# Kernel tuning notes

Hardware: AMD Instinct MI355X
Metric: run time of the kernel (lower is better)

Reference implementation:

```python
import jax, jax.numpy as jnp
import numpy as np

ALPHA = 1.702
LIMIT = 7.0
EPS = 1e-5

E, K, H, I = 8, 2, 2048, 2048
B, S = 1, 1024


def setup_inputs() -> dict:
    key = jax.random.key(0)
    k1, k2, k3, k4, k5 = jax.random.split(key, 5)
    x = jax.random.normal(k1, (B, S, H), dtype=jnp.float32)
    norm_w = jax.random.normal(k2, (H,), dtype=jnp.float32) * 0.02 + 1.0
    router_w = jax.random.normal(k3, (E, H), dtype=jnp.float32) * (1.0 / np.sqrt(H))
    w_gu = jax.random.normal(k4, (E, H, 2 * I), dtype=jnp.float32) * (1.0 / np.sqrt(H))
    w_down = jax.random.normal(k5, (E, I, H), dtype=jnp.float32) * (1.0 / np.sqrt(I))
    return {"x": x, "norm_w": norm_w, "router_w": router_w,
            "w_gu": w_gu, "w_down": w_down, "top_k": K}


def _rmsnorm(x, w):
    var = jnp.mean(x * x, axis=-1, keepdims=True)
    return x * jax.lax.rsqrt(var + EPS) * w


def _swiglu(h):
    # interleaved gate/linear halves, clamped (GPT-OSS style)
    glu = jnp.minimum(h[..., ::2], LIMIT)
    lin = jnp.clip(h[..., 1::2], -LIMIT, LIMIT)
    return glu * jax.nn.sigmoid(ALPHA * glu) * (lin + 1.0)


def reference(x, norm_w, router_w, w_gu, w_down, top_k):
    b, s, h = x.shape
    t = _rmsnorm(x, norm_w).reshape(b * s, h)          # [T, H]
    T = t.shape[0]

    # Router: linear -> softmax -> top-k -> normalize selected affinities
    logits = jnp.einsum('th,eh->te', t, router_w)      # [T, E]
    probs = jax.nn.softmax(logits, axis=-1)
    vals, idx = jax.lax.top_k(probs, top_k)            # [T, K]
    vals = vals / jnp.sum(vals, axis=-1, keepdims=True)
    cw = jnp.zeros_like(probs).at[jnp.arange(T)[:, None], idx].add(vals)  # [T, E]

    # Expert MLPs (dense per-expert reference of the blockwise grouped GEMM)
    hgu = jnp.einsum('th,ehf->etf', t, w_gu)           # [E, T, 2I]
    act = _swiglu(hgu)                                 # [E, T, I]
    oe = jnp.einsum('eti,eio->eto', act, w_down)       # [E, T, H]
    out = jnp.einsum('eto,te->to', oe, cw)             # [T, H]
    return out.reshape(b, s, h)
```

## Files before the change

kernel.cpp:

```cpp
#include <hip/hip_runtime.h>
#include <hip/hip_bf16.h>

#define H_   2048
#define E_   8
#define T_   1024
#define TWOI 4096
#define I_   2048
#define ALPHA 1.702f
#define LIMIT 7.0f

#define BM 128
#define BN 128
#define BKK 32
#define BTW 40

typedef __attribute__((ext_vector_type(8))) short short8;
typedef __attribute__((ext_vector_type(4))) float f32x4;

#define AS3U(p) ((__attribute__((address_space(3))) unsigned int*)(p))
#define AS1U(p) ((const __attribute__((address_space(1))) unsigned int*)(p))

__device__ __forceinline__ unsigned short f2bf(float f) {
    unsigned int u = __float_as_uint(f);
    u += 0x7fff + ((u >> 16) & 1);
    return (unsigned short)(u >> 16);
}

__device__ __forceinline__ unsigned int cvtpk_bf16(float lo, float hi) {
    unsigned int r;
    asm("v_cvt_pk_bf16_f32 %0, %1, %2" : "=v"(r) : "v"(lo), "v"(hi));
    return r;
}

__global__ void zero_counts(int* __restrict__ counts) {
    int i = threadIdx.x;
    if (i < E_) counts[i] = 0;
}

__global__ __launch_bounds__(256) void rms_router(
    const float* __restrict__ x, const float* __restrict__ nw,
    const float* __restrict__ rw,
    unsigned short* __restrict__ tbf, int* __restrict__ counts,
    int* __restrict__ tlist, int* __restrict__ tslot, float* __restrict__ tw)
{
    int t = blockIdx.x;
    int tid = threadIdx.x;
    int wave = tid >> 6, lane = tid & 63;
    const float* xr = x + (size_t)t * H_;

    float4 v0 = *(const float4*)(xr + tid * 4);
    float4 v1 = *(const float4*)(xr + 1024 + tid * 4);
    float ss = v0.x*v0.x + v0.y*v0.y + v0.z*v0.z + v0.w*v0.w
             + v1.x*v1.x + v1.y*v1.y + v1.z*v1.z + v1.w*v1.w;
    #pragma unroll
    for (int s = 32; s; s >>= 1) ss += __shfl_xor(ss, s);

    __shared__ float red[4];
    __shared__ float wlog[4][8];
    if (lane == 0) red[wave] = ss;
    __syncthreads();
    float total = red[0] + red[1] + red[2] + red[3];
    float scale = rsqrtf(total * (1.0f / H_) + 1e-5f);

    float4 n0 = *(const float4*)(nw + tid * 4);
    float4 n1 = *(const float4*)(nw + 1024 + tid * 4);
    float tv[8];
    tv[0] = v0.x * scale * n0.x; tv[1] = v0.y * scale * n0.y;
    tv[2] = v0.z * scale * n0.z; tv[3] = v0.w * scale * n0.w;
    tv[4] = v1.x * scale * n1.x; tv[5] = v1.y * scale * n1.y;
    tv[6] = v1.z * scale * n1.z; tv[7] = v1.w * scale * n1.w;

    ushort4 o0 = make_ushort4(f2bf(tv[0]), f2bf(tv[1]), f2bf(tv[2]), f2bf(tv[3]));
    ushort4 o1 = make_ushort4(f2bf(tv[4]), f2bf(tv[5]), f2bf(tv[6]), f2bf(tv[7]));
    *(ushort4*)(tbf + (size_t)t * H_ + tid * 4) = o0;
    *(ushort4*)(tbf + (size_t)t * H_ + 1024 + tid * 4) = o1;

    float acc[E_];
    #pragma unroll
    for (int e = 0; e < E_; e++) {
        const float* r0 = rw + (size_t)e * H_ + tid * 4;
        float4 a = *(const float4*)r0;
        float4 b = *(const float4*)(r0 + 1024);
        acc[e] = tv[0]*a.x + tv[1]*a.y + tv[2]*a.z + tv[3]*a.w
               + tv[4]*b.x + tv[5]*b.y + tv[6]*b.z + tv[7]*b.w;
    }
    #pragma unroll
    for (int s = 32; s; s >>= 1)
        #pragma unroll
        for (int e = 0; e < E_; e++) acc[e] += __shfl_xor(acc[e], s);
    if (lane == 0)
        #pragma unroll
        for (int e = 0; e < E_; e++) wlog[wave][e] = acc[e];
    __syncthreads();

    if (tid == 0) {
        float lg[E_];
        #pragma unroll
        for (int e = 0; e < E_; e++)
            lg[e] = wlog[0][e] + wlog[1][e] + wlog[2][e] + wlog[3][e];
        int i0 = 0;
        #pragma unroll
        for (int e = 1; e < E_; e++) if (lg[e] > lg[i0]) i0 = e;
        int i1 = -1;
        #pragma unroll
        for (int e = 0; e < E_; e++) {
            if (e == i0) continue;
            if (i1 < 0 || lg[e] > lg[i1]) i1 = e;
        }
        float e1 = expf(lg[i1] - lg[i0]);
        float s = 1.0f + e1;
        float w0 = 1.0f / s, w1 = e1 / s;
        int p0 = atomicAdd(&counts[i0], 1);
        tlist[i0 * T_ + p0] = t; tslot[i0 * T_ + p0] = 0; tw[i0 * T_ + p0] = w0;
        int p1 = atomicAdd(&counts[i1], 1);
        tlist[i1 * T_ + p1] = t; tslot[i1 * T_ + p1] = 1; tw[i1 * T_ + p1] = w1;
    }
}

__device__ __forceinline__ void compute_step(
    const unsigned short (*Asb)[BKK], const unsigned short (*Btb)[BTW],
    int wm, int wn, int lane, f32x4 acc[4][4])
{
    short8 a[4], b[4];
    int arow = wm * 64 + (lane & 15);
    int brow = wn * 64 + (lane & 15);
    int koff = (lane >> 4) * 8;
    #pragma unroll
    for (int mi = 0; mi < 4; mi++)
        a[mi] = *(const short8*)(&Asb[arow + mi * 16][koff]);
    #pragma unroll
    for (int ni = 0; ni < 4; ni++)
        b[ni] = *(const short8*)(&Btb[brow + ni * 16][koff]);
    __builtin_amdgcn_s_setprio(1);
    #pragma unroll
    for (int mi = 0; mi < 4; mi++)
        #pragma unroll
        for (int ni = 0; ni < 4; ni++)
            acc[mi][ni] = __builtin_amdgcn_mfma_f32_16x16x32_bf16(a[mi], b[ni], acc[mi][ni], 0, 0, 0);
    __builtin_amdgcn_s_setprio(0);
}

#define STEP(TT, RCUR, RNEXT, PRE) {                                               \
    if (PRE) {                                                                     \
        int kk2_ = ((TT) + 2) * BKK;                                               \
        __builtin_amdgcn_global_load_lds(AS1U(asrc0 + kk2_), AS3U(&As[c2][wave * 32][0]), 16, 0, 0);      \
        __builtin_amdgcn_global_load_lds(AS1U(asrc1 + kk2_), AS3U(&As[c2][wave * 32 + 16][0]), 16, 0, 0); \
        _Pragma("unroll")                                                          \
        for (int j = 0; j < 16; j++)                                               \
            RNEXT[j] = bcol[(size_t)(kk2_ + sk + j) * ldbv];                       \
    }                                                                              \
    compute_step(As[c0], Bt[(TT) & 1], wm, wn, lane, acc);                         \
    {                                                                              \
        unsigned int pk_[8];                                                       \
        _Pragma("unroll")                                                          \
        for (int h = 0; h < 8; h++) pk_[h] = cvtpk_bf16(RCUR[2 * h], RCUR[2 * h + 1]); \
        unsigned short* db_ = &Bt[((TT) + 1) & 1][sn][sk];                         \
        *(uint4*)(db_)     = make_uint4(pk_[0], pk_[1], pk_[2], pk_[3]);           \
        *(uint4*)(db_ + 8) = make_uint4(pk_[4], pk_[5], pk_[6], pk_[7]);           \
    }                                                                              \
    if (PRE) { asm volatile("s_waitcnt vmcnt(18)" ::: "memory"); }                 \
    else     { asm volatile("s_waitcnt vmcnt(0)"  ::: "memory"); }                 \
    asm volatile("s_waitcnt lgkmcnt(0)" ::: "memory");                             \
    __builtin_amdgcn_sched_barrier(0);                                             \
    __builtin_amdgcn_s_barrier();                                                  \
    __builtin_amdgcn_sched_barrier(0);                                             \
    { int tmp_ = c0; c0 = c1; c1 = c2; c2 = tmp_; }                                \
}

#define GEMM_PIPELINE(NS)                                                          \
    float r0[16], r1[16];                                                          \
    int c0 = 0, c1 = 1, c2 = 2;                                                    \
                                    \
    __builtin_amdgcn_global_load_lds(AS1U(asrc0), AS3U(&As[0][wave * 32][0]), 16, 0, 0);            \
    __builtin_amdgcn_global_load_lds(AS1U(asrc1), AS3U(&As[0][wave * 32 + 16][0]), 16, 0, 0);       \
    _Pragma("unroll")                                                              \
    for (int j = 0; j < 16; j++) r0[j] = bcol[(size_t)(sk + j) * ldbv];            \
    __builtin_amdgcn_global_load_lds(AS1U(asrc0 + BKK), AS3U(&As[1][wave * 32][0]), 16, 0, 0);      \
    __builtin_amdgcn_global_load_lds(AS1U(asrc1 + BKK), AS3U(&As[1][wave * 32 + 16][0]), 16, 0, 0); \
    _Pragma("unroll")                                                              \
    for (int j = 0; j < 16; j++) r1[j] = bcol[(size_t)(BKK + sk + j) * ldbv];      \
    {                                                                              \
        unsigned int pk_[8];                                                       \
        _Pragma("unroll")                                                          \
        for (int h = 0; h < 8; h++) pk_[h] = cvtpk_bf16(r0[2 * h], r0[2 * h + 1]); \
        unsigned short* db_ = &Bt[0][sn][sk];                                      \
        *(uint4*)(db_)     = make_uint4(pk_[0], pk_[1], pk_[2], pk_[3]);           \
        *(uint4*)(db_ + 8) = make_uint4(pk_[4], pk_[5], pk_[6], pk_[7]);           \
    }                                                                              \
    asm volatile("s_waitcnt vmcnt(18)" ::: "memory");                              \
    asm volatile("s_waitcnt lgkmcnt(0)" ::: "memory");                             \
    __builtin_amdgcn_sched_barrier(0);                                             \
    __builtin_amdgcn_s_barrier();                                                  \
    __builtin_amdgcn_sched_barrier(0);                                             \
    for (int t = 0; t < (NS) - 2; t += 2) {                                        \
        STEP(t,     r1, r0, 1)                                                     \
        STEP(t + 1, r0, r1, 1)                                                     \
    }                                                                              \
    STEP((NS) - 2, r1, r0, 0)                                                      \
    compute_step(As[c0], Bt[((NS) - 1) & 1], wm, wn, lane, acc);

__global__ __launch_bounds__(256, 3) void gu_gemm(
    const unsigned short* __restrict__ tbf,
    const float* __restrict__ wgu,
    const int* __restrict__ counts, const int* __restrict__ tlist,
    unsigned short* __restrict__ act)
{
    int bid = blockIdx.x;
    int mtile = bid >> 8;
    int rem = bid & 255;
    int e = rem >> 5;
    int n0 = (rem & 31) * BN;

    int cnt = counts[e];
    int m0 = mtile * BM;
    if (m0 >= cnt) return;

    __shared__ __align__(16) unsigned short As[3][BM][BKK];
    __shared__ __align__(16) unsigned short Bt[2][BN][BTW];

    int tid = threadIdx.x;
    int lane = tid & 63, wave = tid >> 6;
    int wm = wave >> 1, wn = wave & 1;

    int row0 = wave * 32 + (lane >> 2);
    int gr0 = m0 + row0, gr1 = gr0 + 16;
    int tok0 = tlist[e * T_ + (gr0 < cnt ? gr0 : 0)];
    int tok1 = tlist[e * T_ + (gr1 < cnt ? gr1 : 0)];
    const unsigned short* asrc0 = tbf + (size_t)tok0 * H_ + (lane & 3) * 8;
    const unsigned short* asrc1 = tbf + (size_t)tok1 * H_ + (lane & 3) * 8;

    int sn = tid & 127;
    int sk = (tid >> 7) * 16;
    const float* bcol = wgu + (size_t)e * H_ * TWOI + n0 + sn;
    const int ldbv = TWOI;

    f32x4 acc[4][4];
    #pragma unroll
    for (int mi = 0; mi < 4; mi++)
        #pragma unroll
        for (int ni = 0; ni < 4; ni++) acc[mi][ni] = (f32x4){0.f, 0.f, 0.f, 0.f};

    GEMM_PIPELINE(64)

    #pragma unroll
    for (int mi = 0; mi < 4; mi++) {
        #pragma unroll
        for (int ni = 0; ni < 4; ni++) {
            #pragma unroll
            for (int r = 0; r < 4; r++) {
                float v = acc[mi][ni][r];
                float p = __shfl_xor(v, 1);
                int rowe = wm * 64 + mi * 16 + (lane >> 4) * 4 + r;
                int grow = m0 + rowe;
                if (!(lane & 1) && grow < cnt) {
                    float glu = fminf(v, LIMIT);
                    float lin = fminf(fmaxf(p, -LIMIT), LIMIT);
                    float g = glu / (1.0f + __expf(-ALPHA * glu));
                    float a_ = g * (lin + 1.0f);
                    int col = n0 + wn * 64 + ni * 16 + (lane & 15);
                    act[((size_t)e * T_ + grow) * I_ + (col >> 1)] = f2bf(a_);
                }
            }
        }
    }
}

__global__ __launch_bounds__(256, 3) void down_gemm(
    const unsigned short* __restrict__ act,
    const float* __restrict__ wdn,
    const int* __restrict__ counts, const int* __restrict__ tlist,
    const int* __restrict__ tslot, const float* __restrict__ tw,
    float* __restrict__ parts)
{
    int bid = blockIdx.x;
    int mtile = bid >> 8;
    int rem = bid & 255;
    int e = rem >> 5;
    int ks = (rem >> 4) & 1;
    int ntile = rem & 15;
    int n0 = ntile * BN;
    int kbase = ks * (I_ / 2);

    int cnt = counts[e];
    int m0 = mtile * BM;
    if (m0 >= cnt) return;

    __shared__ __align__(16) unsigned short As[3][BM][BKK];
    __shared__ __align__(16) unsigned short Bt[2][BN][BTW];

    int tid = threadIdx.x;
    int lane = tid & 63, wave = tid >> 6;
    int wm = wave >> 1, wn = wave & 1;

    int row0 = wave * 32 + (lane >> 2);
    const unsigned short* asrc0 = act + ((size_t)e * T_ + m0 + row0) * I_ + kbase + (lane & 3) * 8;
    const unsigned short* asrc1 = asrc0 + (size_t)16 * I_;

    int sn = tid & 127;
    int sk = (tid >> 7) * 16;
    const float* bcol = wdn + (size_t)e * I_ * H_ + (size_t)kbase * H_ + n0 + sn;
    const int ldbv = H_;

    f32x4 acc[4][4];
    #pragma unroll
    for (int mi = 0; mi < 4; mi++)
        #pragma unroll
        for (int ni = 0; ni < 4; ni++) acc[mi][ni] = (f32x4){0.f, 0.f, 0.f, 0.f};

    GEMM_PIPELINE(32)

    #pragma unroll
    for (int mi = 0; mi < 4; mi++) {
        int rowe = wm * 64 + mi * 16 + (lane >> 4) * 4;
        int grow0 = m0 + rowe;
        #pragma unroll
        for (int r = 0; r < 4; r++) {
            int grow = grow0 + r;
            if (grow < cnt) {
                int tok  = tlist[e * T_ + grow];
                int slot = tslot[e * T_ + grow];
                float w  = tw[e * T_ + grow];
                float* dst = parts + ((size_t)(ks * 2 + slot) * T_ + tok) * H_;
                #pragma unroll
                for (int ni = 0; ni < 4; ni++) {
                    int col = n0 + wn * 64 + ni * 16 + (lane & 15);
                    dst[col] = w * acc[mi][ni][r];
                }
            }
        }
    }
}

__global__ __launch_bounds__(256) void combine_kernel(
    const float* __restrict__ parts, float* __restrict__ out)
{
    int i = blockIdx.x * blockDim.x + threadIdx.x;
    const float4* p0 = (const float4*)parts;
    const float4* p1 = (const float4*)(parts + (size_t)T_ * H_);
    const float4* p2 = (const float4*)(parts + (size_t)2 * T_ * H_);
    const float4* p3 = (const float4*)(parts + (size_t)3 * T_ * H_);
    float4 a = p0[i], b = p1[i], c = p2[i], d = p3[i];
    float4 s;
    s.x = (a.x + b.x) + (c.x + d.x);
    s.y = (a.y + b.y) + (c.y + d.y);
    s.z = (a.z + b.z) + (c.z + d.z);
    s.w = (a.w + b.w) + (c.w + d.w);
    ((float4*)out)[i] = s;
}

extern "C" void kernel_launch(void* const* d_in, const int* in_sizes, int n_in,
                              void* d_out, int out_size, void* d_ws, size_t ws_size,
                              hipStream_t stream)
{
    const float* x   = (const float*)d_in[0];
    const float* nw  = (const float*)d_in[1];
    const float* rw  = (const float*)d_in[2];
    const float* wgu = (const float*)d_in[3];
    const float* wdn = (const float*)d_in[4];
    float* out = (float*)d_out;

    char* ws = (char*)d_ws;
    unsigned short* tbf = (unsigned short*)ws;
    unsigned short* act = (unsigned short*)(ws + (4u << 20));
    float* parts = (float*)(ws + (36u << 20));
    int*   counts = (int*)(ws + (68u << 20));
    int*   tlist  = (int*)(ws + (68u << 20) + 256);
    int*   tslot  = (int*)(ws + (68u << 20) + 256 + 32 * 1024);
    float* tw     = (float*)(ws + (68u << 20) + 256 + 64 * 1024);

    zero_counts<<<dim3(1), 64, 0, stream>>>(counts);
    rms_router<<<dim3(T_), 256, 0, stream>>>(x, nw, rw, tbf, counts, tlist, tslot, tw);
    gu_gemm<<<dim3(2048), 256, 0, stream>>>(tbf, wgu, counts, tlist, act);
    down_gemm<<<dim3(2048), 256, 0, stream>>>(act, wdn, counts, tlist, tslot, tw, parts);
    combine_kernel<<<dim3((T_ * H_ / 4) / 256), 256, 0, stream>>>(parts, out);
}
```

Before: 190.3 us.

## Split down GEMM K four ways and store bf16 partials for combine

The down-projection GEMM now splits the intermediate dimension into four slices instead of two, doubling the grid so more blocks run on the device. Partial outputs are stored as bf16 instead of fp32, so the eight partial buffers fit in the same workspace and the combine kernel reads them as packed 8-element vectors. The intent is more parallelism in the down GEMM and less partial-buffer traffic. The cost is rounding each partial to bf16 before summing, which loses accuracy, and a combine kernel that now reads eight buffers instead of four.

```diff
diff --git a/kernel.cpp b/kernel.cpp
--- a/kernel.cpp
+++ b/kernel.cpp
@@ -24,6 +24,11 @@
     unsigned int u = __float_as_uint(f);
     u += 0x7fff + ((u >> 16) & 1);
     return (unsigned short)(u >> 16);
+}
+
+__device__ __forceinline__ float bf2f(unsigned short s) {
+    unsigned int u = ((unsigned int)s) << 16;
+    return __uint_as_float(u);
 }
 
 __device__ __forceinline__ unsigned int cvtpk_bf16(float lo, float hi) {
@@ -270,16 +275,16 @@
     const float* __restrict__ wdn,
     const int* __restrict__ counts, const int* __restrict__ tlist,
     const int* __restrict__ tslot, const float* __restrict__ tw,
-    float* __restrict__ parts)
+    unsigned short* __restrict__ parts)
 {
     int bid = blockIdx.x;
-    int mtile = bid >> 8;
-    int rem = bid & 255;
-    int e = rem >> 5;
-    int ks = (rem >> 4) & 1;
+    int mtile = bid >> 9;
+    int rem = bid & 511;
+    int e = rem >> 6;
+    int ks = (rem >> 4) & 3;
     int ntile = rem & 15;
     int n0 = ntile * BN;
-    int kbase = ks * (I_ / 2);
+    int kbase = ks * (I_ / 4);
 
     int cnt = counts[e];
     int m0 = mtile * BM;
@@ -307,7 +312,7 @@
         #pragma unroll
         for (int ni = 0; ni < 4; ni++) acc[mi][ni] = (f32x4){0.f, 0.f, 0.f, 0.f};
 
-    GEMM_PIPELINE(32)
+    GEMM_PIPELINE(16)
 
     #pragma unroll
     for (int mi = 0; mi < 4; mi++) {
@@ -320,11 +325,11 @@
                 int tok  = tlist[e * T_ + grow];
                 int slot = tslot[e * T_ + grow];
                 float w  = tw[e * T_ + grow];
-                float* dst = parts + ((size_t)(ks * 2 + slot) * T_ + tok) * H_;
+                unsigned short* dst = parts + ((size_t)(ks * 2 + slot) * T_ + tok) * H_;
                 #pragma unroll
                 for (int ni = 0; ni < 4; ni++) {
                     int col = n0 + wn * 64 + ni * 16 + (lane & 15);
-                    dst[col] = w * acc[mi][ni][r];
+                    dst[col] = f2bf(w * acc[mi][ni][r]);
                 }
             }
         }
@@ -332,20 +337,24 @@
 }
 
 __global__ __launch_bounds__(256) void combine_kernel(
-    const float* __restrict__ parts, float* __restrict__ out)
+    const unsigned short* __restrict__ parts, float* __restrict__ out)
 {
     int i = blockIdx.x * blockDim.x + threadIdx.x;
-    const float4* p0 = (const float4*)parts;
-    const float4* p1 = (const float4*)(parts + (size_t)T_ * H_);
-    const float4* p2 = (const float4*)(parts + (size_t)2 * T_ * H_);
-    const float4* p3 = (const float4*)(parts + (size_t)3 * T_ * H_);
-    float4 a = p0[i], b = p1[i], c = p2[i], d = p3[i];
-    float4 s;
-    s.x = (a.x + b.x) + (c.x + d.x);
-    s.y = (a.y + b.y) + (c.y + d.y);
-    s.z = (a.z + b.z) + (c.z + d.z);
-    s.w = (a.w + b.w) + (c.w + d.w);
-    ((float4*)out)[i] = s;
+    size_t base = (size_t)i * 8;
+    float s[8];
+    #pragma unroll
+    for (int j = 0; j < 8; j++) s[j] = 0.0f;
+    #pragma unroll
+    for (int p = 0; p < 8; p++) {
+        short8 v = *(const short8*)(parts + (size_t)p * T_ * H_ + base);
+        #pragma unroll
+        for (int j = 0; j < 8; j++)
+            s[j] += bf2f((unsigned short)v[j]);
+    }
+    float4 o0 = make_float4(s[0], s[1], s[2], s[3]);
+    float4 o1 = make_float4(s[4], s[5], s[6], s[7]);
+    *(float4*)(out + base)     = o0;
+    *(float4*)(out + base + 4) = o1;
 }
 
 extern "C" void kernel_launch(void* const* d_in, const int* in_sizes, int n_in,
@@ -362,7 +371,7 @@
     char* ws = (char*)d_ws;
     unsigned short* tbf = (unsigned short*)ws;
     unsigned short* act = (unsigned short*)(ws + (4u << 20));
-    float* parts = (float*)(ws + (36u << 20));
+    unsigned short* parts = (unsigned short*)(ws + (36u << 20));
     int*   counts = (int*)(ws + (68u << 20));
     int*   tlist  = (int*)(ws + (68u << 20) + 256);
     int*   tslot  = (int*)(ws + (68u << 20) + 256 + 32 * 1024);
@@ -371,6 +380,6 @@
     zero_counts<<<dim3(1), 64, 0, stream>>>(counts);
     rms_router<<<dim3(T_), 256, 0, stream>>>(x, nw, rw, tbf, counts, tlist, tslot, tw);
     gu_gemm<<<dim3(2048), 256, 0, stream>>>(tbf, wgu, counts, tlist, act);
-    down_gemm<<<dim3(2048), 256, 0, stream>>>(act, wdn, counts, tlist, tslot, tw, parts);
-    combine_kernel<<<dim3((T_ * H_ / 4) / 256), 256, 0, stream>>>(parts, out);
-}
+    down_gemm<<<dim3(4096), 256, 0, stream>>>(act, wdn, counts, tlist, tslot, tw, parts);
+    combine_kernel<<<dim3((T_ * H_ / 8) / 256), 256, 0, stream>>>(parts, out);
+}
```

New measurement: 203.9 us. +7.2%, slower.
